# Kernel tuning notes

Measured on AMD Instinct MI355X. Metric: run time of the kernel, lower is better.

## Reference

```python
import jax, jax.numpy as jnp
import numpy as np

N_GROUPS = 32
N_HEADS = 16
EPS = 1e-5


def group_norm(x, w, b):
    # x: [B, C, T]
    B, C, T = x.shape
    xg = x.reshape(B, N_GROUPS, C // N_GROUPS, T)
    mu = xg.mean(axis=(2, 3), keepdims=True)
    var = xg.var(axis=(2, 3), keepdims=True)
    xn = ((xg - mu) * jax.lax.rsqrt(var + EPS)).reshape(B, C, T)
    return xn * w[None, :, None] + b[None, :, None]


def setup_inputs() -> dict:
    key = jax.random.key(0)
    ks = jax.random.split(key, 5)
    B, C, T = 4, 1024, 1024
    return {
        "x": jax.random.normal(ks[0], (B, C, T), jnp.float32),
        "norm_weight": jnp.ones((C,), jnp.float32),
        "norm_bias": jnp.zeros((C,), jnp.float32),
        "qkv_w": jax.random.normal(ks[1], (3 * C, C), jnp.float32) * 0.02,
        "qkv_b": jax.random.normal(ks[2], (3 * C,), jnp.float32) * 0.02,
        "proj_w": jax.random.normal(ks[3], (C, C), jnp.float32) * 0.02,
        "proj_b": jax.random.normal(ks[4], (C,), jnp.float32) * 0.02,
    }


def reference(x, norm_weight, norm_bias, qkv_w, qkv_b, proj_w, proj_b):
    B, C, T = x.shape
    H = N_HEADS
    ch = C // H
    # GroupNorm + 1x1 conv to QKV: [B, 3C, T]
    xn = group_norm(x, norm_weight, norm_bias)
    qkv = jnp.einsum('oc,bct->bot', qkv_w, xn) + qkv_b[None, :, None]
    # Legacy layout: [B, H*3*ch, T] -> [B, H, 3, ch, T]
    qkv = qkv.reshape(B, H, 3, ch, T)
    q, k, v = qkv[:, :, 0], qkv[:, :, 1], qkv[:, :, 2]
    scale = 1.0 / jnp.sqrt(jnp.sqrt(jnp.asarray(ch, x.dtype)))
    w = jnp.einsum('bhct,bhcs->bhts', q * scale, k * scale)
    w = jax.nn.softmax(w.astype(jnp.float32), axis=-1).astype(w.dtype)
    a = jnp.einsum('bhts,bhcs->bhct', w, v).reshape(B, C, T)
    h = jnp.einsum('oc,bct->bot', proj_w, a) + proj_b[None, :, None]
    return x + h
```

## Files before the change

kernel.cpp:

```cpp
#include <hip/hip_runtime.h>
#include <hip/hip_bf16.h>

typedef __bf16 bf16;
typedef bf16  bf16x4 __attribute__((ext_vector_type(4)));
typedef bf16  bf16x8 __attribute__((ext_vector_type(8)));
typedef float f32x4  __attribute__((ext_vector_type(4)));

union B8 { bf16x8 v; bf16 e[8]; };
union B4 { bf16x4 v; bf16 e[4]; };
union F4 { f32x4 v; float e[4]; };

#define GLOAD_LDS16(g, l)                                            \
  __builtin_amdgcn_global_load_lds(                                  \
      (const __attribute__((address_space(1))) void*)(g),            \
      (__attribute__((address_space(3))) void*)(l), 16, 0, 0)

#define SWZ(arr, R, c8) (*(const bf16x8*)&(arr)[(size_t)(R) * 64 + (((c8) ^ ((R) & 7)) << 3)])

__global__ __launch_bounds__(256) void conv_w_kernel(
    const float* __restrict__ qkvw, const float* __restrict__ qkvb,
    const float* __restrict__ pw,
    bf16* __restrict__ Wb, bf16* __restrict__ Pb, float* __restrict__ bs)
{
  const int row = blockIdx.x;
  const int tid = threadIdx.x;
  if (row < 3072) {
    const float s = ((row % 192) < 128) ? 0.42468158f : 1.0f;
    const float4 a = ((const float4*)(qkvw + (size_t)row * 1024))[tid];
    B4 o;
    o.e[0] = (bf16)(a.x * s); o.e[1] = (bf16)(a.y * s);
    o.e[2] = (bf16)(a.z * s); o.e[3] = (bf16)(a.w * s);
    ((bf16x4*)(Wb + (size_t)row * 1024))[tid] = o.v;
    if (tid == 0) bs[row] = qkvb[row] * s;
  } else {
    const int r = row - 3072;
    const float4 a = ((const float4*)(pw + (size_t)r * 1024))[tid];
    B4 o;
    o.e[0] = (bf16)a.x; o.e[1] = (bf16)a.y;
    o.e[2] = (bf16)a.z; o.e[3] = (bf16)a.w;
    ((bf16x4*)(Pb + (size_t)r * 1024))[tid] = o.v;
  }
}

__global__ __launch_bounds__(256) void gn_t_kernel(
    const float* __restrict__ x, const float* __restrict__ w,
    const float* __restrict__ bias, bf16* __restrict__ xnt)
{
  const int blk = blockIdx.x;
  const int b = blk >> 5, g = blk & 31;
  const float* xp = x + (size_t)(b * 1024 + g * 32) * 1024;
  const int tid = threadIdx.x;

  float s = 0.f, ss = 0.f;
  for (int ch = tid; ch < 4096; ch += 256) {
    const float4* p = (const float4*)(xp + (size_t)ch * 8);
    float4 u0 = p[0], u1 = p[1];
    s  += u0.x + u0.y + u0.z + u0.w + u1.x + u1.y + u1.z + u1.w;
    ss += u0.x*u0.x + u0.y*u0.y + u0.z*u0.z + u0.w*u0.w
        + u1.x*u1.x + u1.y*u1.y + u1.z*u1.z + u1.w*u1.w;
  }
  #pragma unroll
  for (int m = 1; m < 64; m <<= 1) { s += __shfl_xor(s, m); ss += __shfl_xor(ss, m); }

  __shared__ float red[8];
  __shared__ float stats[2];
  const int wave = tid >> 6, lane = tid & 63;
  if (lane == 0) { red[wave] = s; red[4 + wave] = ss; }
  __syncthreads();
  if (tid == 0) {
    float ts  = red[0] + red[1] + red[2] + red[3];
    float tss = red[4] + red[5] + red[6] + red[7];
    float mu  = ts * (1.f / 32768.f);
    float var = tss * (1.f / 32768.f) - mu * mu;
    stats[0] = mu;
    stats[1] = rsqrtf(var + 1e-5f);
  }
  __syncthreads();
  const float mu = stats[0], rs = stats[1];

  for (int ti = 0; ti < 4; ++ti) {
    const int t = ti * 256 + tid;
    B8 o[4];
    #pragma unroll
    for (int cc = 0; cc < 32; ++cc) {
      const float wt = w[g * 32 + cc] * rs;
      const float bsv = bias[g * 32 + cc];
      const float v = xp[(size_t)cc * 1024 + t];
      o[cc >> 3].e[cc & 7] = (bf16)((v - mu) * wt + bsv);
    }
    bf16* dst = xnt + (size_t)(b * 1024 + t) * 1024 + g * 32;
    #pragma unroll
    for (int j = 0; j < 4; ++j) *(bf16x8*)(dst + j * 8) = o[j].v;
  }
}

__global__ __launch_bounds__(256) void gemm_qkv_kernel(
    const bf16* __restrict__ xnt, const bf16* __restrict__ Wb,
    const float* __restrict__ bs, bf16* __restrict__ qkT, bf16* __restrict__ vv)
{
  const int bx = blockIdx.x;
  const int t0 = blockIdx.y * 128, z = blockIdx.z;
  const bf16* Ab = xnt + (size_t)z * 1024 * 1024;
  const bf16* Bb = Wb + (size_t)bx * 128 * 1024;

  __shared__ __align__(16) bf16 Al[128 * 64];
  __shared__ __align__(16) bf16 Bl[128 * 64];

  const int tid  = threadIdx.x;
  const int wave = tid >> 6, lane = tid & 63;
  const int quad = lane >> 4, l15 = lane & 15;
  const int wr = wave >> 1, wc = wave & 1;
  const int lrow = lane >> 3, lp = lane & 7;

  F4 acc[4][4];
  #pragma unroll
  for (int i = 0; i < 4; ++i)
    #pragma unroll
    for (int j = 0; j < 4; ++j) acc[i][j].v = (f32x4){0.f, 0.f, 0.f, 0.f};

  for (int k0 = 0; k0 < 1024; k0 += 64) {
    #pragma unroll
    for (int call = 0; call < 4; ++call) {
      const int row = wave * 32 + call * 8 + lrow;
      const int c8  = lp ^ (row & 7);
      GLOAD_LDS16(Ab + (size_t)(t0 + row) * 1024 + k0 + c8 * 8,
                  &Al[(wave * 32 + call * 8) * 64]);
      GLOAD_LDS16(Bb + (size_t)row * 1024 + k0 + c8 * 8,
                  &Bl[(wave * 32 + call * 8) * 64]);
    }
    __syncthreads();

    #pragma unroll
    for (int ks = 0; ks < 2; ++ks) {
      bf16x8 af[4], bfr[4];
      #pragma unroll
      for (int mt = 0; mt < 4; ++mt)
        af[mt] = SWZ(Al, wr * 64 + mt * 16 + l15, ks * 4 + quad);
      #pragma unroll
      for (int nt = 0; nt < 4; ++nt)
        bfr[nt] = SWZ(Bl, wc * 64 + nt * 16 + l15, ks * 4 + quad);
      #pragma unroll
      for (int mt = 0; mt < 4; ++mt)
        #pragma unroll
        for (int nt = 0; nt < 4; ++nt)
          acc[mt][nt].v = __builtin_amdgcn_mfma_f32_16x16x32_bf16(
              af[mt], bfr[nt], acc[mt][nt].v, 0, 0, 0);
    }
    __syncthreads();
  }

  #pragma unroll
  for (int nt = 0; nt < 4; ++nt) {
    const int base = bx * 128 + wc * 64 + nt * 16;
    const int r192 = base % 192, head = base / 192;
    const float bb = bs[base + l15];
    if (r192 < 128) {
      const size_t col = head * 128 + r192 + l15;
      #pragma unroll
      for (int mt = 0; mt < 4; ++mt)
        #pragma unroll
        for (int r = 0; r < 4; ++r) {
          const int t = t0 + wr * 64 + mt * 16 + quad * 4 + r;
          qkT[(size_t)(z * 1024 + t) * 2048 + col] = (bf16)(acc[mt][nt].e[r] + bb);
        }
    } else {
      bf16* vrow = vv + ((size_t)z * 1024 + head * 64 + (r192 - 128) + l15) * 1024;
      #pragma unroll
      for (int mt = 0; mt < 4; ++mt)
        #pragma unroll
        for (int r = 0; r < 4; ++r) {
          const int t = t0 + wr * 64 + mt * 16 + quad * 4 + r;
          vrow[t] = (bf16)(acc[mt][nt].e[r] + bb);
        }
    }
  }
}

__global__ __launch_bounds__(256) void gemm_proj_kernel(
    const bf16* __restrict__ Pb, const bf16* __restrict__ Bt,
    float* __restrict__ Cf, const float* __restrict__ bias,
    const float* __restrict__ resf)
{
  const int z = blockIdx.z;
  Bt   += (size_t)z * 1024 * 1024;
  Cf   += (size_t)z * 1024 * 1024;
  resf += (size_t)z * 1024 * 1024;
  const int n0 = blockIdx.x * 128, m0 = blockIdx.y * 64;

  __shared__ __align__(16) bf16 Al[64 * 64];
  __shared__ __align__(16) bf16 Bl[128 * 64];

  const int tid  = threadIdx.x;
  const int wave = tid >> 6, lane = tid & 63;
  const int quad = lane >> 4, l15 = lane & 15;
  const int wr = wave >> 1, wc = wave & 1;
  const int lrow = lane >> 3, lp = lane & 7;

  F4 acc[2][4];
  #pragma unroll
  for (int i = 0; i < 2; ++i)
    #pragma unroll
    for (int j = 0; j < 4; ++j) acc[i][j].v = (f32x4){0.f, 0.f, 0.f, 0.f};

  for (int k0 = 0; k0 < 1024; k0 += 64) {
    #pragma unroll
    for (int call = 0; call < 2; ++call) {
      const int row = wave * 16 + call * 8 + lrow;
      const int c8  = lp ^ (row & 7);
      GLOAD_LDS16(Pb + (size_t)(m0 + row) * 1024 + k0 + c8 * 8,
                  &Al[(wave * 16 + call * 8) * 64]);
    }
    #pragma unroll
    for (int call = 0; call < 4; ++call) {
      const int row = wave * 32 + call * 8 + lrow;
      const int c8  = lp ^ (row & 7);
      GLOAD_LDS16(Bt + (size_t)(n0 + row) * 1024 + k0 + c8 * 8,
                  &Bl[(wave * 32 + call * 8) * 64]);
    }
    __syncthreads();

    #pragma unroll
    for (int ks = 0; ks < 2; ++ks) {
      bf16x8 af[2], bfr[4];
      #pragma unroll
      for (int mt = 0; mt < 2; ++mt)
        af[mt] = SWZ(Al, wr * 32 + mt * 16 + l15, ks * 4 + quad);
      #pragma unroll
      for (int nt = 0; nt < 4; ++nt)
        bfr[nt] = SWZ(Bl, wc * 64 + nt * 16 + l15, ks * 4 + quad);
      #pragma unroll
      for (int mt = 0; mt < 2; ++mt)
        #pragma unroll
        for (int nt = 0; nt < 4; ++nt)
          acc[mt][nt].v = __builtin_amdgcn_mfma_f32_16x16x32_bf16(
              af[mt], bfr[nt], acc[mt][nt].v, 0, 0, 0);
    }
    __syncthreads();
  }

  #pragma unroll
  for (int mt = 0; mt < 2; ++mt) {
    #pragma unroll
    for (int r = 0; r < 4; ++r) {
      const int m = m0 + wr * 32 + mt * 16 + quad * 4 + r;
      const float bb = bias[m];
      #pragma unroll
      for (int nt = 0; nt < 4; ++nt) {
        const int n = n0 + wc * 64 + nt * 16 + l15;
        Cf[(size_t)m * 1024 + n] = acc[mt][nt].e[r] + bb + resf[(size_t)m * 1024 + n];
      }
    }
  }
}

__global__ __launch_bounds__(256) void attn_kernel(
    const bf16* __restrict__ qkTin, const bf16* __restrict__ vmat,
    bf16* __restrict__ aout)
{
  const int h = blockIdx.x, tt = blockIdx.y, z = blockIdx.z;
  const bf16* qk = qkTin + (size_t)z * 1024 * 2048;
  const bf16* vp = vmat + (size_t)z * 1024 * 1024 + (size_t)(h * 64) * 1024;
  aout += (size_t)z * 1024 * 1024;
  const int t0 = tt * 64;

  __shared__ __align__(16) bf16 qP[64 * 64];
  __shared__ __align__(16) bf16 kl[2][64 * 64];
  __shared__ __align__(16) bf16 vl[2][64 * 64];

  const int tid  = threadIdx.x;
  const int wave = tid >> 6, lane = tid & 63;
  const int quad = lane >> 4, l15 = lane & 15;
  const int lrow = lane >> 3, lp = lane & 7;

  const int r0 = wave * 16 + lrow, r1 = wave * 16 + 8 + lrow;
  const int c80 = lp ^ (r0 & 7), c81 = lp ^ (r1 & 7);

  GLOAD_LDS16(qk + (size_t)(t0 + r0) * 2048 + h * 128 + c80 * 8, &qP[(wave * 16) * 64]);
  GLOAD_LDS16(qk + (size_t)(t0 + r1) * 2048 + h * 128 + c81 * 8, &qP[(wave * 16 + 8) * 64]);
  GLOAD_LDS16(qk + (size_t)r0 * 2048 + h * 128 + 64 + c80 * 8, &kl[0][(wave * 16) * 64]);
  GLOAD_LDS16(qk + (size_t)r1 * 2048 + h * 128 + 64 + c81 * 8, &kl[0][(wave * 16 + 8) * 64]);
  GLOAD_LDS16(vp + (size_t)r0 * 1024 + c80 * 8, &vl[0][(wave * 16) * 64]);
  GLOAD_LDS16(vp + (size_t)r1 * 1024 + c81 * 8, &vl[0][(wave * 16 + 8) * 64]);
  __syncthreads();

  const int Rq = wave * 16 + l15;
  const bf16x8 bq0 = SWZ(qP, Rq, quad);
  const bf16x8 bq1 = SWZ(qP, Rq, quad + 4);

  float l_i = 0.f;
  F4 oacc[4];
  #pragma unroll
  for (int ct = 0; ct < 4; ++ct) oacc[ct].v = (f32x4){0.f, 0.f, 0.f, 0.f};

  const int prow = wave * 16 + l15;
  bf16* const pbase = &qP[(size_t)prow * 64];
  const int pq8 = (quad & 1) * 4;

  int buf = 0;
  for (int s0 = 0; s0 < 1024; s0 += 64) {
    if (s0 + 64 < 1024) {
      const int nb = buf ^ 1, sn = s0 + 64;
      GLOAD_LDS16(qk + (size_t)(sn + r0) * 2048 + h * 128 + 64 + c80 * 8,
                  &kl[nb][(wave * 16) * 64]);
      GLOAD_LDS16(qk + (size_t)(sn + r1) * 2048 + h * 128 + 64 + c81 * 8,
                  &kl[nb][(wave * 16 + 8) * 64]);
      GLOAD_LDS16(vp + (size_t)r0 * 1024 + sn + c80 * 8, &vl[nb][(wave * 16) * 64]);
      GLOAD_LDS16(vp + (size_t)r1 * 1024 + sn + c81 * 8, &vl[nb][(wave * 16 + 8) * 64]);
    }

    F4 sacc[4];
    #pragma unroll
    for (int st = 0; st < 4; ++st) sacc[st].v = (f32x4){0.f, 0.f, 0.f, 0.f};
    #pragma unroll
    for (int st = 0; st < 4; ++st) {
      const int Rk = st * 16 + l15;
      const bf16x8 ak0 = SWZ(kl[buf], Rk, quad);
      const bf16x8 ak1 = SWZ(kl[buf], Rk, quad + 4);
      sacc[st].v = __builtin_amdgcn_mfma_f32_16x16x32_bf16(ak0, bq0, sacc[st].v, 0, 0, 0);
      sacc[st].v = __builtin_amdgcn_mfma_f32_16x16x32_bf16(ak1, bq1, sacc[st].v, 0, 0, 0);
    }

    #pragma unroll
    for (int st = 0; st < 4; ++st) {
      B4 pk;
      #pragma unroll
      for (int r = 0; r < 4; ++r) {
        const float p = __builtin_amdgcn_exp2f(sacc[st].e[r]);
        l_i += p;
        pk.e[r] = (bf16)p;
      }
      const int c8 = (st * 2 + (quad >> 1)) ^ (prow & 7);
      *(bf16x4*)(pbase + (c8 << 3) + pq8) = pk.v;
    }

    #pragma unroll
    for (int ks = 0; ks < 2; ++ks) {
      const bf16x8 ap = SWZ(qP, prow, ks * 4 + quad);
      #pragma unroll
      for (int ct = 0; ct < 4; ++ct) {
        const bf16x8 bv = SWZ(vl[buf], ct * 16 + l15, ks * 4 + quad);
        oacc[ct].v = __builtin_amdgcn_mfma_f32_16x16x32_bf16(ap, bv, oacc[ct].v, 0, 0, 0);
      }
    }
    __syncthreads();
    buf ^= 1;
  }

  l_i += __shfl_xor(l_i, 16);
  l_i += __shfl_xor(l_i, 32);
  const float inv = 1.f / l_i;
  float iv[4];
  #pragma unroll
  for (int r = 0; r < 4; ++r) iv[r] = __shfl(inv, quad * 4 + r);
  #pragma unroll
  for (int r = 0; r < 4; ++r) {
    const int t = t0 + wave * 16 + quad * 4 + r;
    #pragma unroll
    for (int ct = 0; ct < 4; ++ct)
      aout[(size_t)t * 1024 + h * 64 + ct * 16 + l15] = (bf16)(oacc[ct].e[r] * iv[r]);
  }
}

extern "C" void kernel_launch(void* const* d_in, const int* in_sizes, int n_in,
                              void* d_out, int out_size, void* d_ws, size_t ws_size,
                              hipStream_t stream)
{
  const float* x    = (const float*)d_in[0];
  const float* nw   = (const float*)d_in[1];
  const float* nb   = (const float*)d_in[2];
  const float* qkvw = (const float*)d_in[3];
  const float* qkvb = (const float*)d_in[4];
  const float* pw   = (const float*)d_in[5];
  const float* pb   = (const float*)d_in[6];
  float* out = (float*)d_out;

  const long M1 = 1024L * 1024L;
  bf16*  xnt = (bf16*)d_ws;
  bf16*  qkT = xnt + 4 * M1;
  bf16*  vv  = xnt + 12 * M1;
  bf16*  at  = xnt + 16 * M1;
  bf16*  Wb  = xnt + 20 * M1;
  bf16*  Pb  = xnt + 23 * M1;
  float* bs  = (float*)(xnt + 24 * M1);

  conv_w_kernel<<<dim3(4096), dim3(256), 0, stream>>>(qkvw, qkvb, pw, Wb, Pb, bs);
  gn_t_kernel<<<dim3(128), dim3(256), 0, stream>>>(x, nw, nb, xnt);
  gemm_qkv_kernel<<<dim3(24, 8, 4), dim3(256), 0, stream>>>(xnt, Wb, bs, qkT, vv);
  attn_kernel<<<dim3(16, 16, 4), dim3(256), 0, stream>>>(qkT, vv, at);
  gemm_proj_kernel<<<dim3(8, 16, 4), dim3(256), 0, stream>>>(Pb, at, out, pb, x);
}
```

Baseline: 192.0 us.

## Widen attention query tile, shrink proj GEMM tile, vectorize V stores

```diff
diff --git a/kernel.cpp b/kernel.cpp
--- a/kernel.cpp
+++ b/kernel.cpp
@@ -166,12 +166,13 @@
     } else {
       bf16* vrow = vv + ((size_t)z * 1024 + head * 64 + (r192 - 128) + l15) * 1024;
       #pragma unroll
-      for (int mt = 0; mt < 4; ++mt)
-        #pragma unroll
-        for (int r = 0; r < 4; ++r) {
-          const int t = t0 + wr * 64 + mt * 16 + quad * 4 + r;
-          vrow[t] = (bf16)(acc[mt][nt].e[r] + bb);
-        }
+      for (int mt = 0; mt < 4; ++mt) {
+        const int t = t0 + wr * 64 + mt * 16 + quad * 4;
+        B4 pk;
+        #pragma unroll
+        for (int r = 0; r < 4; ++r) pk.e[r] = (bf16)(acc[mt][nt].e[r] + bb);
+        *(bf16x4*)&vrow[t] = pk.v;
+      }
     }
   }
 }
@@ -185,10 +186,10 @@
   Bt   += (size_t)z * 1024 * 1024;
   Cf   += (size_t)z * 1024 * 1024;
   resf += (size_t)z * 1024 * 1024;
-  const int n0 = blockIdx.x * 128, m0 = blockIdx.y * 64;
+  const int n0 = blockIdx.x * 64, m0 = blockIdx.y * 64;
 
   __shared__ __align__(16) bf16 Al[64 * 64];
-  __shared__ __align__(16) bf16 Bl[128 * 64];
+  __shared__ __align__(16) bf16 Bl[64 * 64];
 
   const int tid  = threadIdx.x;
   const int wave = tid >> 6, lane = tid & 63;
@@ -196,11 +197,11 @@
   const int wr = wave >> 1, wc = wave & 1;
   const int lrow = lane >> 3, lp = lane & 7;
 
-  F4 acc[2][4];
+  F4 acc[2][2];
   #pragma unroll
   for (int i = 0; i < 2; ++i)
     #pragma unroll
-    for (int j = 0; j < 4; ++j) acc[i][j].v = (f32x4){0.f, 0.f, 0.f, 0.f};
+    for (int j = 0; j < 2; ++j) acc[i][j].v = (f32x4){0.f, 0.f, 0.f, 0.f};
 
   for (int k0 = 0; k0 < 1024; k0 += 64) {
     #pragma unroll
@@ -209,29 +210,24 @@
       const int c8  = lp ^ (row & 7);
       GLOAD_LDS16(Pb + (size_t)(m0 + row) * 1024 + k0 + c8 * 8,
                   &Al[(wave * 16 + call * 8) * 64]);
-    }
-    #pragma unroll
-    for (int call = 0; call < 4; ++call) {
-      const int row = wave * 32 + call * 8 + lrow;
-      const int c8  = lp ^ (row & 7);
       GLOAD_LDS16(Bt + (size_t)(n0 + row) * 1024 + k0 + c8 * 8,
-                  &Bl[(wave * 32 + call * 8) * 64]);
+                  &Bl[(wave * 16 + call * 8) * 64]);
     }
     __syncthreads();
 
     #pragma unroll
     for (int ks = 0; ks < 2; ++ks) {
-      bf16x8 af[2], bfr[4];
+      bf16x8 af[2], bfr[2];
       #pragma unroll
       for (int mt = 0; mt < 2; ++mt)
         af[mt] = SWZ(Al, wr * 32 + mt * 16 + l15, ks * 4 + quad);
       #pragma unroll
-      for (int nt = 0; nt < 4; ++nt)
-        bfr[nt] = SWZ(Bl, wc * 64 + nt * 16 + l15, ks * 4 + quad);
+      for (int nt = 0; nt < 2; ++nt)
+        bfr[nt] = SWZ(Bl, wc * 32 + nt * 16 + l15, ks * 4 + quad);
       #pragma unroll
       for (int mt = 0; mt < 2; ++mt)
         #pragma unroll
-        for (int nt = 0; nt < 4; ++nt)
+        for (int nt = 0; nt < 2; ++nt)
           acc[mt][nt].v = __builtin_amdgcn_mfma_f32_16x16x32_bf16(
               af[mt], bfr[nt], acc[mt][nt].v, 0, 0, 0);
     }
@@ -245,8 +241,8 @@
       const int m = m0 + wr * 32 + mt * 16 + quad * 4 + r;
       const float bb = bias[m];
       #pragma unroll
-      for (int nt = 0; nt < 4; ++nt) {
-        const int n = n0 + wc * 64 + nt * 16 + l15;
+      for (int nt = 0; nt < 2; ++nt) {
+        const int n = n0 + wc * 32 + nt * 16 + l15;
         Cf[(size_t)m * 1024 + n] = acc[mt][nt].e[r] + bb + resf[(size_t)m * 1024 + n];
       }
     }
@@ -261,9 +257,9 @@
   const bf16* qk = qkTin + (size_t)z * 1024 * 2048;
   const bf16* vp = vmat + (size_t)z * 1024 * 1024 + (size_t)(h * 64) * 1024;
   aout += (size_t)z * 1024 * 1024;
-  const int t0 = tt * 64;
-
-  __shared__ __align__(16) bf16 qP[64 * 64];
+  const int t0 = tt * 128;
+
+  __shared__ __align__(16) bf16 qP[128 * 64];
   __shared__ __align__(16) bf16 kl[2][64 * 64];
   __shared__ __align__(16) bf16 vl[2][64 * 64];
 
@@ -272,28 +268,38 @@
   const int quad = lane >> 4, l15 = lane & 15;
   const int lrow = lane >> 3, lp = lane & 7;
 
+  #pragma unroll
+  for (int c = 0; c < 4; ++c) {
+    const int row = wave * 32 + c * 8 + lrow;
+    const int c8  = lp ^ (row & 7);
+    GLOAD_LDS16(qk + (size_t)(t0 + row) * 2048 + h * 128 + c8 * 8,
+                &qP[(wave * 32 + c * 8) * 64]);
+  }
   const int r0 = wave * 16 + lrow, r1 = wave * 16 + 8 + lrow;
   const int c80 = lp ^ (r0 & 7), c81 = lp ^ (r1 & 7);
-
-  GLOAD_LDS16(qk + (size_t)(t0 + r0) * 2048 + h * 128 + c80 * 8, &qP[(wave * 16) * 64]);
-  GLOAD_LDS16(qk + (size_t)(t0 + r1) * 2048 + h * 128 + c81 * 8, &qP[(wave * 16 + 8) * 64]);
   GLOAD_LDS16(qk + (size_t)r0 * 2048 + h * 128 + 64 + c80 * 8, &kl[0][(wave * 16) * 64]);
   GLOAD_LDS16(qk + (size_t)r1 * 2048 + h * 128 + 64 + c81 * 8, &kl[0][(wave * 16 + 8) * 64]);
   GLOAD_LDS16(vp + (size_t)r0 * 1024 + c80 * 8, &vl[0][(wave * 16) * 64]);
   GLOAD_LDS16(vp + (size_t)r1 * 1024 + c81 * 8, &vl[0][(wave * 16 + 8) * 64]);
   __syncthreads();
 
-  const int Rq = wave * 16 + l15;
-  const bf16x8 bq0 = SWZ(qP, Rq, quad);
-  const bf16x8 bq1 = SWZ(qP, Rq, quad + 4);
-
-  float l_i = 0.f;
-  F4 oacc[4];
-  #pragma unroll
-  for (int ct = 0; ct < 4; ++ct) oacc[ct].v = (f32x4){0.f, 0.f, 0.f, 0.f};
-
-  const int prow = wave * 16 + l15;
-  bf16* const pbase = &qP[(size_t)prow * 64];
+  bf16x8 bq0[2], bq1[2];
+  int prow[2];
+  #pragma unroll
+  for (int b = 0; b < 2; ++b) {
+    const int Rq = wave * 32 + b * 16 + l15;
+    bq0[b] = SWZ(qP, Rq, quad);
+    bq1[b] = SWZ(qP, Rq, quad + 4);
+    prow[b] = Rq;
+  }
+
+  float l_i[2] = {0.f, 0.f};
+  F4 oacc[2][4];
+  #pragma unroll
+  for (int b = 0; b < 2; ++b)
+    #pragma unroll
+    for (int ct = 0; ct < 4; ++ct) oacc[b][ct].v = (f32x4){0.f, 0.f, 0.f, 0.f};
+
   const int pq8 = (quad & 1) * 4;
 
   int buf = 0;
@@ -308,56 +314,73 @@
       GLOAD_LDS16(vp + (size_t)r1 * 1024 + sn + c81 * 8, &vl[nb][(wave * 16 + 8) * 64]);
     }
 
-    F4 sacc[4];
-    #pragma unroll
-    for (int st = 0; st < 4; ++st) sacc[st].v = (f32x4){0.f, 0.f, 0.f, 0.f};
+    bf16x8 ak0[4], ak1[4], bv[2][4];
     #pragma unroll
     for (int st = 0; st < 4; ++st) {
       const int Rk = st * 16 + l15;
-      const bf16x8 ak0 = SWZ(kl[buf], Rk, quad);
-      const bf16x8 ak1 = SWZ(kl[buf], Rk, quad + 4);
-      sacc[st].v = __builtin_amdgcn_mfma_f32_16x16x32_bf16(ak0, bq0, sacc[st].v, 0, 0, 0);
-      sacc[st].v = __builtin_amdgcn_mfma_f32_16x16x32_bf16(ak1, bq1, sacc[st].v, 0, 0, 0);
-    }
-
-    #pragma unroll
-    for (int st = 0; st < 4; ++st) {
-      B4 pk;
-      #pragma unroll
-      for (int r = 0; r < 4; ++r) {
-        const float p = __builtin_amdgcn_exp2f(sacc[st].e[r]);
-        l_i += p;
-        pk.e[r] = (bf16)p;
+      ak0[st] = SWZ(kl[buf], Rk, quad);
+      ak1[st] = SWZ(kl[buf], Rk, quad + 4);
+    }
+    #pragma unroll
+    for (int ks = 0; ks < 2; ++ks)
+      #pragma unroll
+      for (int ct = 0; ct < 4; ++ct)
+        bv[ks][ct] = SWZ(vl[buf], ct * 16 + l15, ks * 4 + quad);
+
+    #pragma unroll
+    for (int b = 0; b < 2; ++b) {
+      F4 sacc[4];
+      #pragma unroll
+      for (int st = 0; st < 4; ++st) sacc[st].v = (f32x4){0.f, 0.f, 0.f, 0.f};
+      #pragma unroll
+      for (int st = 0; st < 4; ++st) {
+        sacc[st].v = __builtin_amdgcn_mfma_f32_16x16x32_bf16(ak0[st], bq0[b], sacc[st].v, 0, 0, 0);
+        sacc[st].v = __builtin_amdgcn_mfma_f32_16x16x32_bf16(ak1[st], bq1[b], sacc[st].v, 0, 0, 0);
       }
-      const int c8 = (st * 2 + (quad >> 1)) ^ (prow & 7);
-      *(bf16x4*)(pbase + (c8 << 3) + pq8) = pk.v;
-    }
-
-    #pragma unroll
-    for (int ks = 0; ks < 2; ++ks) {
-      const bf16x8 ap = SWZ(qP, prow, ks * 4 + quad);
-      #pragma unroll
-      for (int ct = 0; ct < 4; ++ct) {
-        const bf16x8 bv = SWZ(vl[buf], ct * 16 + l15, ks * 4 + quad);
-        oacc[ct].v = __builtin_amdgcn_mfma_f32_16x16x32_bf16(ap, bv, oacc[ct].v, 0, 0, 0);
+
+      bf16* const pbase = &qP[(size_t)prow[b] * 64];
+      #pragma unroll
+      for (int st = 0; st < 4; ++st) {
+        B4 pk;
+        #pragma unroll
+        for (int r = 0; r < 4; ++r) {
+          const float p = __builtin_amdgcn_exp2f(sacc[st].e[r]);
+          l_i[b] += p;
+          pk.e[r] = (bf16)p;
+        }
+        const int c8 = (st * 2 + (quad >> 1)) ^ (prow[b] & 7);
+        *(bf16x4*)(pbase + (c8 << 3) + pq8) = pk.v;
+      }
+
+      #pragma unroll
+      for (int ks = 0; ks < 2; ++ks) {
+        const bf16x8 ap = SWZ(qP, prow[b], ks * 4 + quad);
+        #pragma unroll
+        for (int ct = 0; ct < 4; ++ct)
+          oacc[b][ct].v = __builtin_amdgcn_mfma_f32_16x16x32_bf16(
+              ap, bv[ks][ct], oacc[b][ct].v, 0, 0, 0);
       }
     }
     __syncthreads();
     buf ^= 1;
   }
 
-  l_i += __shfl_xor(l_i, 16);
-  l_i += __shfl_xor(l_i, 32);
-  const float inv = 1.f / l_i;
-  float iv[4];
-  #pragma unroll
-  for (int r = 0; r < 4; ++r) iv[r] = __shfl(inv, quad * 4 + r);
-  #pragma unroll
-  for (int r = 0; r < 4; ++r) {
-    const int t = t0 + wave * 16 + quad * 4 + r;
-    #pragma unroll
-    for (int ct = 0; ct < 4; ++ct)
-      aout[(size_t)t * 1024 + h * 64 + ct * 16 + l15] = (bf16)(oacc[ct].e[r] * iv[r]);
+  #pragma unroll
+  for (int b = 0; b < 2; ++b) {
+    float li = l_i[b];
+    li += __shfl_xor(li, 16);
+    li += __shfl_xor(li, 32);
+    const float inv = 1.f / li;
+    float iv[4];
+    #pragma unroll
+    for (int r = 0; r < 4; ++r) iv[r] = __shfl(inv, quad * 4 + r);
+    #pragma unroll
+    for (int r = 0; r < 4; ++r) {
+      const int t = t0 + wave * 32 + b * 16 + quad * 4 + r;
+      #pragma unroll
+      for (int ct = 0; ct < 4; ++ct)
+        aout[(size_t)t * 1024 + h * 64 + ct * 16 + l15] = (bf16)(oacc[b][ct].e[r] * iv[r]);
+    }
   }
 }
 
@@ -386,6 +409,6 @@
   conv_w_kernel<<<dim3(4096), dim3(256), 0, stream>>>(qkvw, qkvb, pw, Wb, Pb, bs);
   gn_t_kernel<<<dim3(128), dim3(256), 0, stream>>>(x, nw, nb, xnt);
   gemm_qkv_kernel<<<dim3(24, 8, 4), dim3(256), 0, stream>>>(xnt, Wb, bs, qkT, vv);
-  attn_kernel<<<dim3(16, 16, 4), dim3(256), 0, stream>>>(qkT, vv, at);
-  gemm_proj_kernel<<<dim3(8, 16, 4), dim3(256), 0, stream>>>(Pb, at, out, pb, x);
-}
+  attn_kernel<<<dim3(16, 8, 4), dim3(256), 0, stream>>>(qkT, vv, at);
+  gemm_proj_kernel<<<dim3(16, 16, 4), dim3(256), 0, stream>>>(Pb, at, out, pb, x);
+}
```

Result: faster. 186.1 us (-3.1%).
